# Performance work log

Hardware: AMD Instinct MI355X
Metric: run time of the kernel (lower is better)

Reference implementation:

```python
import jax, jax.numpy as jnp
import numpy as np

# RBF_Conv2d config (matches init_kwargs)
KH = KW = 3
STRIDE = 1
OUT_CH = 256
IN_CH = 64
STD = 2.0  # gauss RBF std (activate_param[0])


def setup_inputs() -> dict:
    key = jax.random.key(0)
    k1, k2 = jax.random.split(key)
    x = jax.random.normal(k1, (16, IN_CH, 56, 56), dtype=jnp.float32)
    # kaiming_uniform_ on fan_in = IN_CH*KH*KW = 576 -> bound = sqrt(6/576)
    bound = float(np.sqrt(6.0 / (IN_CH * KH * KW)))
    weight = jax.random.uniform(k2, (OUT_CH, IN_CH * KH * KW), dtype=jnp.float32,
                                minval=-bound, maxval=bound)
    return {"x": x, "weight": weight}


def _cdist_conv(x, weight):
    # im2col: [B, C*KH*KW, Ho, Wo]; channel ordering (c, kh, kw) matches F.unfold
    patches = jax.lax.conv_general_dilated_patches(
        x, (KH, KW), (STRIDE, STRIDE), 'VALID')
    B, Kdim, Ho, Wo = patches.shape
    win = patches.reshape(B, Kdim, Ho * Wo).transpose(0, 2, 1)  # [B, P, K]
    # Euclidean distance via the expansion ||w||^2 + ||c||^2 - 2 w.c (no [B,P,K,O] tensor)
    w2 = jnp.sum(win * win, axis=-1, keepdims=True)            # [B, P, 1]
    c2 = jnp.sum(weight * weight, axis=-1)[None, None, :]      # [1, 1, O]
    d2 = w2 + c2 - 2.0 * jnp.einsum('bpk,ok->bpo', win, weight)
    dist = jnp.sqrt(jnp.maximum(d2, 1e-12))                    # [B, P, O]
    return dist, (B, Ho, Wo)


def reference(x, weight):
    dist, (B, Ho, Wo) = _cdist_conv(x, weight)
    # gauss RBF: exp(-d^2 / (2*std^2))
    act = jnp.exp(-(dist * dist) / (2.0 * STD * STD))
    # permute back to [B, O, Ho, Wo] like the torch code
    return act.transpose(0, 2, 1).reshape(B, OUT_CH, Ho, Wo)
```

## Files before the change

kernel.cpp:

```cpp
#include <hip/hip_runtime.h>
#include <hip/hip_bf16.h>
#include <stdint.h>

#define BATCH 16
#define IN_CH 64
#define HIN 56
#define WIN_ 56
#define HO 54
#define WO 54
#define P_PER_B (HO*WO)
#define P_PAD 2944
#define OUT_CH 256
#define KDIM 576
#define NPIX (HIN*WIN_)

typedef __attribute__((ext_vector_type(8))) short short8;
typedef __attribute__((ext_vector_type(4))) float f32x4;

__device__ __forceinline__ unsigned short f2bf(float f) {
    unsigned int u = __float_as_uint(f);
    unsigned int r = (u + 0x7fffu + ((u >> 16) & 1u)) >> 16;
    return (unsigned short)r;
}


__global__ void prep_weight(const float* __restrict__ w, short* __restrict__ wbf,
                            float* __restrict__ c2) {
    int o = blockIdx.x;
    int lane = threadIdx.x;
    float s = 0.f;
    #pragma unroll
    for (int j = 0; j < 9; ++j) {
        int k = j * 64 + lane;
        int c = k / 9, tap = k % 9;
        float v = w[o * KDIM + k];
        s += v * v;
        ((unsigned short*)wbf)[o * KDIM + tap * 64 + c] = f2bf(v);
    }
    #pragma unroll
    for (int off = 32; off > 0; off >>= 1) s += __shfl_down(s, off);
    if (lane == 0) c2[o] = s;
}

__global__ __launch_bounds__(256) void transpose_kernel(
    const float* __restrict__ x, short* __restrict__ xT, float* __restrict__ s) {
    __shared__ short lds[64 * 65];
    __shared__ float red[256];
    const int b    = blockIdx.x / 49;
    const int pix0 = (blockIdx.x % 49) * 64;
    const int tid  = threadIdx.x;
    const int quarter = tid >> 6;
    const int pix  = tid & 63;
    const float* xb = x + (size_t)b * IN_CH * NPIX + pix0 + pix;
    float acc = 0.f;
    #pragma unroll
    for (int it = 0; it < 16; ++it) {
        int c = quarter * 16 + it;
        float v = xb[c * NPIX];
        acc += v * v;
        lds[pix * 65 + c] = (short)f2bf(v);
    }
    red[tid] = acc;
    __syncthreads();
    const int cs = tid & 63;
    short* xTb = xT + ((size_t)b * NPIX + pix0) * 64;
    #pragma unroll
    for (int it = 0; it < 16; ++it) {
        int pixs = quarter * 16 + it;
        xTb[(size_t)pixs * 64 + cs] = lds[pixs * 65 + cs];
    }
    if (tid < 64)
        s[b * NPIX + pix0 + tid] = red[tid] + red[64 + tid] + red[128 + tid] + red[192 + tid];
}

__global__ void w2_kernel(const float* __restrict__ s, float* __restrict__ w2) {
    int t = blockIdx.x * 256 + threadIdx.x;
    if (t >= BATCH * P_PER_B) return;
    int b = t / P_PER_B, p = t % P_PER_B;
    int oh = p / WO, ow = p % WO;
    const float* sp = s + b * NPIX + oh * WIN_ + ow;
    float acc = 0.f;
    #pragma unroll
    for (int kh = 0; kh < 3; ++kh)
        #pragma unroll
        for (int kw = 0; kw < 3; ++kw)
            acc += sp[kh * WIN_ + kw];
    w2[b * P_PAD + p] = acc;
}


#define AS1(p) ((const __attribute__((address_space(1))) void*)(p))
#define AS3(p) ((__attribute__((address_space(3))) void*)(p))

__constant__ int dtab[9] = {0, 1, 2, 56, 57, 58, 112, 113, 114};

__global__ __launch_bounds__(256) void gemm_rbf(
    const short* __restrict__ xT, const short* __restrict__ wbf,
    const float* __restrict__ w2, const float* __restrict__ c2,
    float* __restrict__ out) {
    __shared__ __align__(16) short lds_a[128 * 64];
    __shared__ __align__(16) short lds_b[128 * 64];

    const int mt = blockIdx.x;
    const int b  = mt / 23;
    const int p0 = (mt % 23) * 128;
    const int n0 = blockIdx.y * 128;

    const int tid  = threadIdx.x;
    const int wave = tid >> 6;
    const int lane = tid & 63;
    const int r16  = lane & 15;
    const int quad = lane >> 4;
    const int wm = (wave >> 1) * 64;
    const int wn = (wave & 1) * 64;

    const int srow = lane >> 3;
    const int scx  = (lane & 7) ^ srow;

    const short* xTb = xT + (size_t)b * NPIX * 64;

    const short* gaB[4];
    const short* gbB[4];
    #pragma unroll
    for (int i = 0; i < 4; ++i) {
        int row = (wave * 4 + i) * 8 + srow;
        int p = p0 + row;
        if (p > P_PER_B - 1) p = P_PER_B - 1;
        int oh = p / WO, ow = p - oh * WO;
        gaB[i] = xTb + (size_t)(oh * WIN_ + ow) * 64 + scx * 8;
        gbB[i] = wbf + (size_t)(n0 + row) * KDIM + scx * 8;
    }
    const int xq = r16 & 7;

    f32x4 acc[4][4];
    #pragma unroll
    for (int i = 0; i < 4; ++i)
        #pragma unroll
        for (int j = 0; j < 4; ++j)
            acc[i][j] = (f32x4){0.f, 0.f, 0.f, 0.f};

    #pragma unroll
    for (int kt = 0; kt < 9; ++kt) {
        const int doff = dtab[kt];
        #pragma unroll
        for (int i = 0; i < 4; ++i) {
            int rb = wave * 4 + i;
            __builtin_amdgcn_global_load_lds(AS1(gaB[i] + doff * 64),
                                             AS3(lds_a + rb * 512), 16, 0, 0);
            __builtin_amdgcn_global_load_lds(AS1(gbB[i] + kt * 64),
                                             AS3(lds_b + rb * 512), 16, 0, 0);
        }
        __syncthreads();
        #pragma unroll
        for (int ks = 0; ks < 2; ++ks) {
            short8 af[4], bfr[4];
            #pragma unroll
            for (int ms = 0; ms < 4; ++ms)
                af[ms] = *(const short8*)(lds_a + (wm + ms * 16 + r16) * 64
                                                + (((ks * 4 + quad) ^ xq) * 8));
            #pragma unroll
            for (int ns = 0; ns < 4; ++ns)
                bfr[ns] = *(const short8*)(lds_b + (wn + ns * 16 + r16) * 64
                                                 + (((ks * 4 + quad) ^ xq) * 8));
            #pragma unroll
            for (int ms = 0; ms < 4; ++ms)
                #pragma unroll
                for (int ns = 0; ns < 4; ++ns)
                    acc[ms][ns] = __builtin_amdgcn_mfma_f32_16x16x32_bf16(
                        af[ms], bfr[ns], acc[ms][ns], 0, 0, 0);
        }
        __syncthreads();
    }

    #pragma unroll
    for (int ms = 0; ms < 4; ++ms) {
        int pl = wm + ms * 16 + quad * 4;
        int p  = p0 + pl;
        if (p >= P_PER_B) continue;
        f32x4 w2v = *(const f32x4*)(w2 + b * P_PAD + p);
        bool full = (p + 3 < P_PER_B);
        #pragma unroll
        for (int ns = 0; ns < 4; ++ns) {
            int o = n0 + wn + ns * 16 + r16;
            float c2o = c2[o];
            f32x4 v;
            #pragma unroll
            for (int r = 0; r < 4; ++r) {
                float d2 = w2v[r] + c2o - 2.0f * acc[ms][ns][r];
                d2 = fmaxf(d2, 1e-12f);
                v[r] = __expf(-0.125f * d2);
            }
            float* outp = out + ((size_t)(b * OUT_CH + o)) * P_PER_B + p;
            if (full) {
                *(f32x4*)outp = v;
            } else {
                #pragma unroll
                for (int r = 0; r < 4; ++r)
                    if (p + r < P_PER_B) outp[r] = v[r];
            }
        }
    }
}


extern "C" void kernel_launch(void* const* d_in, const int* in_sizes, int n_in,
                              void* d_out, int out_size, void* d_ws, size_t ws_size,
                              hipStream_t stream) {
    const float* x = (const float*)d_in[0];
    const float* w = (const float*)d_in[1];
    float* out = (float*)d_out;

    char* ws = (char*)d_ws;
    const size_t wbf_bytes = (size_t)OUT_CH * KDIM * 2;
    const size_t c2_bytes  = 1024;
    const size_t w2_bytes  = (size_t)BATCH * P_PAD * 4;
    const size_t s_bytes   = (size_t)BATCH * NPIX * 4;
    short* wbf = (short*)ws;
    float* c2  = (float*)(ws + wbf_bytes);
    float* w2  = (float*)(ws + wbf_bytes + c2_bytes);
    float* s   = (float*)(ws + wbf_bytes + c2_bytes + w2_bytes);
    short* xT  = (short*)(ws + wbf_bytes + c2_bytes + w2_bytes + s_bytes);

    hipLaunchKernelGGL(prep_weight, dim3(OUT_CH), dim3(64), 0, stream, w, wbf, c2);
    hipLaunchKernelGGL(transpose_kernel, dim3(16 * 49), dim3(256), 0, stream, x, xT, s);
    hipLaunchKernelGGL(w2_kernel, dim3((BATCH * P_PER_B + 255) / 256), dim3(256), 0, stream, s, w2);
    hipLaunchKernelGGL(gemm_rbf, dim3(23 * BATCH, OUT_CH / 128), dim3(256), 0, stream,
                       xT, wbf, w2, c2, out);
}
```

Measured before the change: 104.2 us.

## Stage input halo tile in LDS once and double-buffer weight tiles

Each GEMM block now loads the whole span of input pixels its 128 outputs touch (352 rows of 64 channels) into LDS once. The nine 3x3 taps are then served by shifted LDS reads, instead of issuing nine separate global loads of the A tile. Weight tiles are double-buffered, so the next tap's B tile is fetched while the current one is consumed. This drops one barrier per iteration, and s_setprio is raised around the MFMA section. The per-batch xT stride is padded so the halo reads stay in bounds. LDS use grows to about 77KB per block, which can lower occupancy.

```diff
diff --git a/kernel.cpp b/kernel.cpp
--- a/kernel.cpp
+++ b/kernel.cpp
@@ -13,6 +13,7 @@
 #define OUT_CH 256
 #define KDIM 576
 #define NPIX (HIN*WIN_)
+#define XT_PIX 3264
 
 typedef __attribute__((ext_vector_type(8))) short short8;
 typedef __attribute__((ext_vector_type(4))) float f32x4;
@@ -63,7 +64,7 @@
     red[tid] = acc;
     __syncthreads();
     const int cs = tid & 63;
-    short* xTb = xT + ((size_t)b * NPIX + pix0) * 64;
+    short* xTb = xT + ((size_t)b * XT_PIX + pix0) * 64;
     #pragma unroll
     for (int it = 0; it < 16; ++it) {
         int pixs = quarter * 16 + it;
@@ -92,14 +93,12 @@
 #define AS1(p) ((const __attribute__((address_space(1))) void*)(p))
 #define AS3(p) ((__attribute__((address_space(3))) void*)(p))
 
-__constant__ int dtab[9] = {0, 1, 2, 56, 57, 58, 112, 113, 114};
-
 __global__ __launch_bounds__(256) void gemm_rbf(
     const short* __restrict__ xT, const short* __restrict__ wbf,
     const float* __restrict__ w2, const float* __restrict__ c2,
     float* __restrict__ out) {
-    __shared__ __align__(16) short lds_a[128 * 64];
-    __shared__ __align__(16) short lds_b[128 * 64];
+    __shared__ __align__(16) short lds_a[352 * 64];
+    __shared__ __align__(16) short lds_b[2 * 128 * 64];
 
     const int mt = blockIdx.x;
     const int b  = mt / 23;
@@ -114,21 +113,35 @@
     const int wm = (wave >> 1) * 64;
     const int wn = (wave & 1) * 64;
 
+    const int oh_base  = p0 / WO;
+    const int ihw_base = oh_base * WIN_;
+
     const int srow = lane >> 3;
     const int scx  = (lane & 7) ^ srow;
 
-    const short* xTb = xT + (size_t)b * NPIX * 64;
-
-    const short* gaB[4];
+    const short* aSrc = xT + ((size_t)b * XT_PIX + ihw_base + srow) * 64 + scx * 8;
+    #pragma unroll
+    for (int i = 0; i < 11; ++i) {
+        int rb8 = (wave * 11 + i) * 8;
+        __builtin_amdgcn_global_load_lds(AS1(aSrc + (size_t)rb8 * 64),
+                                         AS3(lds_a + rb8 * 64), 16, 0, 0);
+    }
     const short* gbB[4];
     #pragma unroll
     for (int i = 0; i < 4; ++i) {
         int row = (wave * 4 + i) * 8 + srow;
-        int p = p0 + row;
+        gbB[i] = wbf + (size_t)(n0 + row) * KDIM + scx * 8;
+        __builtin_amdgcn_global_load_lds(AS1(gbB[i]),
+                                         AS3(lds_b + (wave * 4 + i) * 512), 16, 0, 0);
+    }
+
+    int ihw_rel[4];
+    #pragma unroll
+    for (int ms = 0; ms < 4; ++ms) {
+        int p = p0 + wm + ms * 16 + r16;
         if (p > P_PER_B - 1) p = P_PER_B - 1;
         int oh = p / WO, ow = p - oh * WO;
-        gaB[i] = xTb + (size_t)(oh * WIN_ + ow) * 64 + scx * 8;
-        gbB[i] = wbf + (size_t)(n0 + row) * KDIM + scx * 8;
+        ihw_rel[ms] = oh * WIN_ + ow - ihw_base;
     }
     const int xq = r16 & 7;
 
@@ -139,29 +152,34 @@
         for (int j = 0; j < 4; ++j)
             acc[i][j] = (f32x4){0.f, 0.f, 0.f, 0.f};
 
+    __syncthreads();
+
+    constexpr int dtab_l[9] = {0, 1, 2, 56, 57, 58, 112, 113, 114};
     #pragma unroll
     for (int kt = 0; kt < 9; ++kt) {
-        const int doff = dtab[kt];
-        #pragma unroll
-        for (int i = 0; i < 4; ++i) {
-            int rb = wave * 4 + i;
-            __builtin_amdgcn_global_load_lds(AS1(gaB[i] + doff * 64),
-                                             AS3(lds_a + rb * 512), 16, 0, 0);
-            __builtin_amdgcn_global_load_lds(AS1(gbB[i] + kt * 64),
-                                             AS3(lds_b + rb * 512), 16, 0, 0);
+        if (kt < 8) {
+            short* dstB = lds_b + ((kt + 1) & 1) * (128 * 64);
+            #pragma unroll
+            for (int i = 0; i < 4; ++i)
+                __builtin_amdgcn_global_load_lds(AS1(gbB[i] + (kt + 1) * 64),
+                                                 AS3(dstB + (wave * 4 + i) * 512), 16, 0, 0);
         }
-        __syncthreads();
+        const short* lb = lds_b + (kt & 1) * (128 * 64);
+        const int dt = dtab_l[kt];
+        __builtin_amdgcn_s_setprio(1);
         #pragma unroll
         for (int ks = 0; ks < 2; ++ks) {
             short8 af[4], bfr[4];
             #pragma unroll
-            for (int ms = 0; ms < 4; ++ms)
-                af[ms] = *(const short8*)(lds_a + (wm + ms * 16 + r16) * 64
-                                                + (((ks * 4 + quad) ^ xq) * 8));
+            for (int ms = 0; ms < 4; ++ms) {
+                int rl = ihw_rel[ms] + dt;
+                af[ms] = *(const short8*)(lds_a + rl * 64
+                                                + (((ks * 4 + quad) ^ (rl & 7)) * 8));
+            }
             #pragma unroll
             for (int ns = 0; ns < 4; ++ns)
-                bfr[ns] = *(const short8*)(lds_b + (wn + ns * 16 + r16) * 64
-                                                 + (((ks * 4 + quad) ^ xq) * 8));
+                bfr[ns] = *(const short8*)(lb + (wn + ns * 16 + r16) * 64
+                                              + (((ks * 4 + quad) ^ xq) * 8));
             #pragma unroll
             for (int ms = 0; ms < 4; ++ms)
                 #pragma unroll
@@ -169,7 +187,8 @@
                     acc[ms][ns] = __builtin_amdgcn_mfma_f32_16x16x32_bf16(
                         af[ms], bfr[ns], acc[ms][ns], 0, 0, 0);
         }
-        __syncthreads();
+        __builtin_amdgcn_s_setprio(0);
+        if (kt < 8) __syncthreads();
     }
 
     #pragma unroll
```

After: 112.3 us. +7.8%, slower.
